# Performance work log

Hardware: AMD Instinct MI355X
Metric: run time of the kernel (lower is better)

Reference implementation:

```python
import jax, jax.numpy as jnp
import numpy as np

NEG_SLOPE = 0.2
EPS = 1e-16  # PyG softmax denominator epsilon


def gat_conv(x, edge_index, W, a_src, a_dst, bias):
    """PyG GATConv, heads=1, concat=True, add_self_loops=True, edge_dim=None."""
    N = x.shape[0]
    h = x @ W  # [N, d]
    loops = jnp.arange(N)
    src = jnp.concatenate([edge_index[0], loops])  # [E+N]
    dst = jnp.concatenate([edge_index[1], loops])
    # per-node attention dot-products, gathered per edge
    s = h @ a_src  # [N]
    t = h @ a_dst  # [N]
    e = jax.nn.leaky_relu(s[src] + t[dst], NEG_SLOPE)  # [E+N]
    # segment softmax over incoming edges of each dst node
    m = jax.ops.segment_max(e, dst, num_segments=N)
    ex = jnp.exp(e - m[dst])
    denom = jax.ops.segment_sum(ex, dst, num_segments=N)
    alpha = ex / (denom[dst] + EPS)  # [E+N]
    out = jax.ops.segment_sum(h[src] * alpha[:, None], dst, num_segments=N)
    return out + bias


def setup_inputs() -> dict:
    key = jax.random.key(0)
    N, E, D, DE = 50000, 600000, 128, 16
    ks = jax.random.split(key, 12)
    scale = 1.0 / np.sqrt(D)
    return {
        "x_one": jax.random.normal(ks[0], (N, D), jnp.float32),
        "edge_index_one": jax.random.randint(ks[1], (2, E), 0, N, jnp.int64),
        "edge_attr_emb_one": jax.random.normal(ks[2], (E, DE), jnp.float32),
        "x_two": jax.random.normal(ks[3], (N, D), jnp.float32),
        "edge_index_two": jax.random.randint(ks[4], (2, E), 0, N, jnp.int64),
        "edge_attr_emb_two": jax.random.normal(ks[5], (E, DE), jnp.float32),
        "W1": jax.random.normal(ks[6], (D, D), jnp.float32) * scale,
        "a_src1": jax.random.normal(ks[7], (D,), jnp.float32) * scale,
        "a_dst1": jax.random.normal(ks[8], (D,), jnp.float32) * scale,
        "b1": jnp.zeros((D,), jnp.float32),
        "W2": jax.random.normal(ks[9], (D, D), jnp.float32) * scale,
        "a_src2": jax.random.normal(ks[10], (D,), jnp.float32) * scale,
        "a_dst2": jax.random.normal(ks[11], (D,), jnp.float32) * scale,
        "b2": jnp.zeros((D,), jnp.float32),
    }


def reference(x_one, edge_index_one, edge_attr_emb_one,
              x_two, edge_index_two, edge_attr_emb_two,
              W1, a_src1, a_dst1, b1, W2, a_src2, a_dst2, b2):
    # edge_attr is ignored: GATConv was built without edge_dim.
    # F.dropout(training=False) is identity in eval mode.
    out_one = jax.nn.relu(gat_conv(x_one, edge_index_one, W1, a_src1, a_dst1, b1))
    out_two = jax.nn.relu(gat_conv(x_two, edge_index_two, W2, a_src2, a_dst2, b2))
    return (out_one, out_two)
```

## Files before the change

### kernel.cpp

```cpp
#include <hip/hip_runtime.h>
#include <math.h>

#define D 128
#define NEG_SLOPE 0.2f
#define EPS 1e-16f
#define PT 4096
#define SCAP 1024
#define CSRCAP (SCAP + 64)

typedef __attribute__((ext_vector_type(8))) __bf16 bf16x8;
typedef __attribute__((ext_vector_type(4))) float f32x4;
typedef __attribute__((ext_vector_type(2))) float f32x2;

__device__ __forceinline__ unsigned short f2bf(float f) {
    return __builtin_bit_cast(unsigned short, (__bf16)f);
}
__device__ __forceinline__ unsigned long long pack4bf(float a, float b, float c, float d) {
    return (unsigned long long)f2bf(a)
         | ((unsigned long long)f2bf(b) << 16)
         | ((unsigned long long)f2bf(c) << 32)
         | ((unsigned long long)f2bf(d) << 48);
}
__device__ __forceinline__ f32x2 bf2f2(unsigned u) {
    f32x2 r;
    r.x = __uint_as_float(u << 16);
    r.y = __uint_as_float(u & 0xffff0000u);
    return r;
}

__global__ __launch_bounds__(256) void k_gemm(const float* __restrict__ X0,
                                              const float* __restrict__ X1,
                                              const float* __restrict__ W0,
                                              const float* __restrict__ W1,
                                              const float* __restrict__ as0,
                                              const float* __restrict__ as1,
                                              const float* __restrict__ ad0,
                                              const float* __restrict__ ad1,
                                              unsigned short* __restrict__ Hb,
                                              float* __restrict__ sv,
                                              float* __restrict__ tv, int N, int nb) {
    __shared__ char lds[65536];
    const int t = threadIdx.x;
    const int g = (blockIdx.x >= nb) ? 1 : 0;
    const int row0 = (blockIdx.x - g * nb) * 128;
    const float* X = g ? X1 : X0;
    const float* W = g ? W1 : W0;
    const float* a_src = g ? as1 : as0;
    const float* a_dst = g ? ad1 : ad0;
    const int gbase = g * N;

    {
        const int n = t & 127;
        const int khalf = (t >> 7) * 64;
        #pragma unroll 4
        for (int i = 0; i < 16; ++i) {
            const int k0 = khalf + i * 4;
            float f0 = W[(size_t)(k0 + 0) * D + n];
            float f1 = W[(size_t)(k0 + 1) * D + n];
            float f2 = W[(size_t)(k0 + 2) * D + n];
            float f3 = W[(size_t)(k0 + 3) * D + n];
            int off = (n * 256 + k0 * 2) ^ ((n & 7) << 4);
            *(unsigned long long*)(lds + 32768 + off) = pack4bf(f0, f1, f2, f3);
        }
    }
    {
        const int c = t & 31;
        #pragma unroll 4
        for (int p = 0; p < 16; ++p) {
            const int m = p * 8 + (t >> 5);
            const int gr = row0 + m;
            float4 v = make_float4(0.f, 0.f, 0.f, 0.f);
            if (gr < N) v = ((const float4*)X)[(size_t)gr * 32 + c];
            int off = (m * 256 + c * 8) ^ ((m & 7) << 4);
            *(unsigned long long*)(lds + off) = pack4bf(v.x, v.y, v.z, v.w);
        }
    }
    __syncthreads();

    const int w = t >> 6;
    const int l = t & 63;
    const int lr = l & 15;
    const int lg = l >> 4;

    f32x4 acc[2][8];
    #pragma unroll
    for (int r = 0; r < 2; ++r)
        #pragma unroll
        for (int nt = 0; nt < 8; ++nt) acc[r][nt] = (f32x4){0.f, 0.f, 0.f, 0.f};

    #pragma unroll
    for (int kk = 0; kk < 4; ++kk) {
        const int kByte = kk * 64 + lg * 16;
        const int m0 = w * 32 + lr;
        const int m1 = m0 + 16;
        bf16x8 a0 = *(const bf16x8*)(lds + ((m0 * 256 + kByte) ^ ((m0 & 7) << 4)));
        bf16x8 a1 = *(const bf16x8*)(lds + ((m1 * 256 + kByte) ^ ((m1 & 7) << 4)));
        #pragma unroll
        for (int nt = 0; nt < 8; ++nt) {
            const int n = nt * 16 + lr;
            bf16x8 b = *(const bf16x8*)(lds + 32768 + ((n * 256 + kByte) ^ ((n & 7) << 4)));
            acc[0][nt] = __builtin_amdgcn_mfma_f32_16x16x32_bf16(a0, b, acc[0][nt], 0, 0, 0);
            acc[1][nt] = __builtin_amdgcn_mfma_f32_16x16x32_bf16(a1, b, acc[1][nt], 0, 0, 0);
        }
    }

    float asv[8], adv[8];
    #pragma unroll
    for (int nt = 0; nt < 8; ++nt) {
        asv[nt] = a_src[nt * 16 + lr];
        adv[nt] = a_dst[nt * 16 + lr];
    }
    #pragma unroll
    for (int r = 0; r < 2; ++r) {
        #pragma unroll
        for (int reg = 0; reg < 4; ++reg) {
            const int row = row0 + w * 32 + r * 16 + lg * 4 + reg;
            float ss = 0.f, tt = 0.f;
            #pragma unroll
            for (int nt = 0; nt < 8; ++nt) {
                float hv = acc[r][nt][reg];
                ss += hv * asv[nt];
                tt += hv * adv[nt];
                if (row < N) Hb[(size_t)(gbase + row) * D + nt * 16 + lr] = f2bf(hv);
            }
            #pragma unroll
            for (int off = 8; off; off >>= 1) {
                ss += __shfl_xor(ss, off);
                tt += __shfl_xor(tt, off);
            }
            if (lr == 0 && row < N) { sv[gbase + row] = ss; tv[gbase + row] = tt; }
        }
    }
}

__global__ __launch_bounds__(256) void k_fill(int* __restrict__ fill, int NSB) {
    int i = blockIdx.x * 256 + threadIdx.x;
    if (i < NSB) fill[i] = i * SCAP;
}

__global__ __launch_bounds__(256) void k_part(const int* __restrict__ s0,
                                              const int* __restrict__ d0,
                                              const int* __restrict__ s1,
                                              const int* __restrict__ d1,
                                              int* __restrict__ fill,
                                              unsigned* __restrict__ P,
                                              int E0, int Et, int N, int NSB) {
    __shared__ int hcnt[2048];
    __shared__ int hbase[2048];
    const int t = threadIdx.x;
    const int i0 = blockIdx.x * PT;
    const int i1 = min(i0 + PT, Et);
    for (int i = t; i < NSB; i += 256) hcnt[i] = 0;
    __syncthreads();
    for (int i = i0 + t; i < i1; i += 256) {
        int dd = (i < E0) ? d0[i] : d1[i - E0] + N;
        atomicAdd(&hcnt[dd >> 6], 1);
    }
    __syncthreads();
    for (int i = t; i < NSB; i += 256) {
        int c = hcnt[i];
        hbase[i] = c ? atomicAdd(&fill[i], c) : 0;
        hcnt[i] = 0;
    }
    __syncthreads();
    for (int i = i0 + t; i < i1; i += 256) {
        int ss, dd;
        if (i < E0) { ss = s0[i]; dd = d0[i]; }
        else        { ss = s1[i - E0] + N; dd = d1[i - E0] + N; }
        int sb = dd >> 6;
        int pos = hbase[sb] + atomicAdd(&hcnt[sb], 1);
        if (pos < (sb + 1) * SCAP)
            P[pos] = (unsigned)ss | ((unsigned)(dd & 63) << 26);
    }
}

__global__ __launch_bounds__(256) void k_gatherf(const unsigned* __restrict__ P,
                                                 const int* __restrict__ fill,
                                                 const float* __restrict__ sv,
                                                 const float* __restrict__ tv,
                                                 const unsigned short* __restrict__ Hb,
                                                 const float* __restrict__ b0,
                                                 const float* __restrict__ b1,
                                                 float* __restrict__ out, int N, int M) {
    __shared__ int cnt[64];
    __shared__ int rp[65];
    __shared__ float dsum[64];
    __shared__ float tvl[64];
    __shared__ int cw[CSRCAP];
    __shared__ unsigned short plb[CSRCAP];
    const int t = threadIdx.x;
    const int sb = blockIdx.x;
    const int bstart = sb * SCAP;
    int bend = fill[sb];
    if (bend > bstart + SCAP) bend = bstart + SCAP;
    const int dbase = sb << 6;

    if (t < 64) {
        cnt[t] = 1;
        int d = dbase + t;
        tvl[t] = (d < M) ? tv[d] : 0.f;
    }
    __syncthreads();
    for (int i = bstart + t; i < bend; i += 256)
        atomicAdd(&cnt[(P[i] >> 26) & 63], 1);
    __syncthreads();
    if (t < 64) {
        int v = cnt[t];
        int inc = v;
        #pragma unroll
        for (int off = 1; off < 64; off <<= 1) {
            int x = __shfl_up(inc, off);
            if (t >= off) inc += x;
        }
        rp[t + 1] = inc;
        if (t == 0) rp[0] = 0;
        int st = inc - v;
        cnt[t] = st + 1;
        int d = dbase + t;
        if (d < M) {
            float es = sv[d] + tvl[t];
            es = (es > 0.f) ? es : NEG_SLOPE * es;
            unsigned short pb = f2bf(__expf(es));
            cw[st] = d;
            plb[st] = pb;
            dsum[t] = __uint_as_float((unsigned)pb << 16);
        } else {
            cw[st] = 0;
            plb[st] = 0;
            dsum[t] = 1.f;
        }
    }
    __syncthreads();
    for (int i = bstart + t; i < bend; i += 256) {
        unsigned w = P[i];
        int dlo = (int)(w >> 26) & 63;
        int src = (int)(w & 0x03FFFFFFu);
        float e = sv[src] + tvl[dlo];
        e = (e > 0.f) ? e : NEG_SLOPE * e;
        unsigned short pb = f2bf(__expf(e));
        int pos = atomicAdd(&cnt[dlo], 1);
        cw[pos] = src;
        plb[pos] = pb;
        atomicAdd(&dsum[dlo], __uint_as_float((unsigned)pb << 16));
    }
    __syncthreads();

    const int wv = t >> 6;
    const int lane = t & 63;
    const int qtr = lane >> 4;
    const int sl = lane & 15;

    for (int q = 0; q < 16; ++q) {
        const int ld = wv * 16 + q;
        const int d = dbase + ld;
        if (d >= M) break;
        const int start = rp[ld];
        const int dg = rp[ld + 1] - start;

        f32x2 a0 = {0.f, 0.f}, a1 = {0.f, 0.f}, a2 = {0.f, 0.f}, a3 = {0.f, 0.f};
        int j = qtr;
        for (; j + 12 < dg; j += 16) {
            const int e0 = start + j;
            int sA = cw[e0];
            int sB = cw[e0 + 4];
            int sC = cw[e0 + 8];
            int sD = cw[e0 + 12];
            float pA = __uint_as_float((unsigned)plb[e0] << 16);
            float pB = __uint_as_float((unsigned)plb[e0 + 4] << 16);
            float pC = __uint_as_float((unsigned)plb[e0 + 8] << 16);
            float pD = __uint_as_float((unsigned)plb[e0 + 12] << 16);
            uint4 wA = *(const uint4*)(Hb + (size_t)sA * D + sl * 8);
            uint4 wB = *(const uint4*)(Hb + (size_t)sB * D + sl * 8);
            uint4 wC = *(const uint4*)(Hb + (size_t)sC * D + sl * 8);
            uint4 wD = *(const uint4*)(Hb + (size_t)sD * D + sl * 8);
            a0 += pA * bf2f2(wA.x); a1 += pA * bf2f2(wA.y); a2 += pA * bf2f2(wA.z); a3 += pA * bf2f2(wA.w);
            a0 += pB * bf2f2(wB.x); a1 += pB * bf2f2(wB.y); a2 += pB * bf2f2(wB.z); a3 += pB * bf2f2(wB.w);
            a0 += pC * bf2f2(wC.x); a1 += pC * bf2f2(wC.y); a2 += pC * bf2f2(wC.z); a3 += pC * bf2f2(wC.w);
            a0 += pD * bf2f2(wD.x); a1 += pD * bf2f2(wD.y); a2 += pD * bf2f2(wD.z); a3 += pD * bf2f2(wD.w);
        }
        for (; j < dg; j += 4) {
            const int e0 = start + j;
            int sA = cw[e0];
            float pA = __uint_as_float((unsigned)plb[e0] << 16);
            uint4 wA = *(const uint4*)(Hb + (size_t)sA * D + sl * 8);
            a0 += pA * bf2f2(wA.x); a1 += pA * bf2f2(wA.y); a2 += pA * bf2f2(wA.z); a3 += pA * bf2f2(wA.w);
        }

        #pragma unroll
        for (int off = 16; off <= 32; off <<= 1) {
            a0.x += __shfl_xor(a0.x, off); a0.y += __shfl_xor(a0.y, off);
            a1.x += __shfl_xor(a1.x, off); a1.y += __shfl_xor(a1.y, off);
            a2.x += __shfl_xor(a2.x, off); a2.y += __shfl_xor(a2.y, off);
            a3.x += __shfl_xor(a3.x, off); a3.y += __shfl_xor(a3.y, off);
        }

        if (qtr == 0) {
            const float* bp = ((d < N) ? b0 : b1) + sl * 8;
            float inv = 1.0f / (dsum[ld] + EPS);
            float4 o0, o1;
            o0.x = fmaxf(a0.x * inv + bp[0], 0.f);
            o0.y = fmaxf(a0.y * inv + bp[1], 0.f);
            o0.z = fmaxf(a1.x * inv + bp[2], 0.f);
            o0.w = fmaxf(a1.y * inv + bp[3], 0.f);
            o1.x = fmaxf(a2.x * inv + bp[4], 0.f);
            o1.y = fmaxf(a2.y * inv + bp[5], 0.f);
            o1.z = fmaxf(a3.x * inv + bp[6], 0.f);
            o1.w = fmaxf(a3.y * inv + bp[7], 0.f);
            float4* op = (float4*)(out + (size_t)d * D + sl * 8);
            op[0] = o0;
            op[1] = o1;
        }
    }
}

static inline size_t rup(size_t x) { return (x + 255) & ~(size_t)255; }

extern "C" void kernel_launch(void* const* d_in, const int* in_sizes, int n_in,
                              void* d_out, int out_size, void* d_ws, size_t ws_size,
                              hipStream_t stream) {
    const int N = in_sizes[0] / D;
    const int M = 2 * N;
    const int E0 = in_sizes[1] / 2;
    const int E1 = in_sizes[4] / 2;
    const int Et = E0 + E1;
    const int NSB = (M + 63) >> 6;
    float* out = (float*)d_out;

    char* ws = (char*)d_ws;
    unsigned short* Hb = (unsigned short*)ws; ws += rup((size_t)M * D * sizeof(unsigned short));
    float* sv = (float*)ws;       ws += rup((size_t)M * sizeof(float));
    float* tv = (float*)ws;       ws += rup((size_t)M * sizeof(float));
    int* fill = (int*)ws;         ws += rup((size_t)NSB * sizeof(int));
    unsigned* P = (unsigned*)ws;

    const int* EI0 = (const int*)d_in[1];
    const int* EI1 = (const int*)d_in[4];
    const int* s0 = EI0, *d0 = EI0 + E0;
    const int* s1 = EI1, *d1 = EI1 + E1;

    const int nb = (N + 127) / 128;

    k_gemm<<<2 * nb, 256, 0, stream>>>((const float*)d_in[0], (const float*)d_in[3],
                                       (const float*)d_in[6], (const float*)d_in[10],
                                       (const float*)d_in[7], (const float*)d_in[11],
                                       (const float*)d_in[8], (const float*)d_in[12],
                                       Hb, sv, tv, N, nb);
    k_fill<<<(NSB + 255) / 256, 256, 0, stream>>>(fill, NSB);
    k_part<<<(Et + PT - 1) / PT, 256, 0, stream>>>(s0, d0, s1, d1, fill, P, E0, Et, N, NSB);
    k_gatherf<<<NSB, 256, 0, stream>>>(P, fill, sv, tv, Hb,
                                       (const float*)d_in[9], (const float*)d_in[13],
                                       out, N, M);
}
```

Baseline: 119.3 us.

## Halve destination buckets, fuse fill into GEMM, pack fp32 edge weights

Destination super-buckets shrink from 64 to 32 nodes with half the capacity, which doubles the number of gather blocks (more parallelism and less LDS per block). The partition tile grows to 8192 edges, so fewer k_part blocks each do more atomic base reservations. The separate fill-init kernel is folded into the GEMM kernel, removing one launch. Edge source index and weight are now packed together as fp32 uint2 in LDS instead of bf16-rounded weights in a separate array. The exchange is more LDS traffic per edge, and the smaller 512-entry buckets can overflow for high in-degree nodes.

```diff
diff --git a/kernel.cpp b/kernel.cpp
--- a/kernel.cpp
+++ b/kernel.cpp
@@ -4,9 +4,10 @@
 #define D 128
 #define NEG_SLOPE 0.2f
 #define EPS 1e-16f
-#define PT 4096
-#define SCAP 1024
-#define CSRCAP (SCAP + 64)
+#define PT 8192
+#define SBSH 5
+#define SCAP 512
+#define CSRCAP (SCAP + 32)
 
 typedef __attribute__((ext_vector_type(8))) __bf16 bf16x8;
 typedef __attribute__((ext_vector_type(4))) float f32x4;
@@ -38,9 +39,15 @@
                                               const float* __restrict__ ad1,
                                               unsigned short* __restrict__ Hb,
                                               float* __restrict__ sv,
-                                              float* __restrict__ tv, int N, int nb) {
+                                              float* __restrict__ tv,
+                                              int* __restrict__ fill,
+                                              int N, int nb, int NSB) {
     __shared__ char lds[65536];
     const int t = threadIdx.x;
+    {
+        int gi = blockIdx.x * 256 + t;
+        if (gi < NSB) fill[gi] = gi * SCAP;
+    }
     const int g = (blockIdx.x >= nb) ? 1 : 0;
     const int row0 = (blockIdx.x - g * nb) * 128;
     const float* X = g ? X1 : X0;
@@ -133,11 +140,6 @@
     }
 }
 
-__global__ __launch_bounds__(256) void k_fill(int* __restrict__ fill, int NSB) {
-    int i = blockIdx.x * 256 + threadIdx.x;
-    if (i < NSB) fill[i] = i * SCAP;
-}
-
 __global__ __launch_bounds__(256) void k_part(const int* __restrict__ s0,
                                               const int* __restrict__ d0,
                                               const int* __restrict__ s1,
@@ -145,8 +147,8 @@
                                               int* __restrict__ fill,
                                               unsigned* __restrict__ P,
                                               int E0, int Et, int N, int NSB) {
-    __shared__ int hcnt[2048];
-    __shared__ int hbase[2048];
+    __shared__ int hcnt[3200];
+    __shared__ int hbase[3200];
     const int t = threadIdx.x;
     const int i0 = blockIdx.x * PT;
     const int i1 = min(i0 + PT, Et);
@@ -154,7 +156,7 @@
     __syncthreads();
     for (int i = i0 + t; i < i1; i += 256) {
         int dd = (i < E0) ? d0[i] : d1[i - E0] + N;
-        atomicAdd(&hcnt[dd >> 6], 1);
+        atomicAdd(&hcnt[dd >> SBSH], 1);
     }
     __syncthreads();
     for (int i = t; i < NSB; i += 256) {
@@ -167,10 +169,10 @@
         int ss, dd;
         if (i < E0) { ss = s0[i]; dd = d0[i]; }
         else        { ss = s1[i - E0] + N; dd = d1[i - E0] + N; }
-        int sb = dd >> 6;
+        int sb = dd >> SBSH;
         int pos = hbase[sb] + atomicAdd(&hcnt[sb], 1);
         if (pos < (sb + 1) * SCAP)
-            P[pos] = (unsigned)ss | ((unsigned)(dd & 63) << 26);
+            P[pos] = (unsigned)ss | ((unsigned)(dd & 31) << 27);
     }
 }
 
@@ -182,33 +184,32 @@
                                                  const float* __restrict__ b0,
                                                  const float* __restrict__ b1,
                                                  float* __restrict__ out, int N, int M) {
-    __shared__ int cnt[64];
-    __shared__ int rp[65];
-    __shared__ float dsum[64];
-    __shared__ float tvl[64];
-    __shared__ int cw[CSRCAP];
-    __shared__ unsigned short plb[CSRCAP];
+    __shared__ int cnt[32];
+    __shared__ int rp[33];
+    __shared__ float dsum[32];
+    __shared__ float tvl[32];
+    __shared__ uint2 ep[CSRCAP];
     const int t = threadIdx.x;
     const int sb = blockIdx.x;
     const int bstart = sb * SCAP;
     int bend = fill[sb];
     if (bend > bstart + SCAP) bend = bstart + SCAP;
-    const int dbase = sb << 6;
-
-    if (t < 64) {
+    const int dbase = sb << SBSH;
+
+    if (t < 32) {
         cnt[t] = 1;
         int d = dbase + t;
         tvl[t] = (d < M) ? tv[d] : 0.f;
     }
     __syncthreads();
     for (int i = bstart + t; i < bend; i += 256)
-        atomicAdd(&cnt[(P[i] >> 26) & 63], 1);
-    __syncthreads();
-    if (t < 64) {
+        atomicAdd(&cnt[P[i] >> 27], 1);
+    __syncthreads();
+    if (t < 32) {
         int v = cnt[t];
         int inc = v;
         #pragma unroll
-        for (int off = 1; off < 64; off <<= 1) {
+        for (int off = 1; off < 32; off <<= 1) {
             int x = __shfl_up(inc, off);
             if (t >= off) inc += x;
         }
@@ -220,28 +221,25 @@
         if (d < M) {
             float es = sv[d] + tvl[t];
             es = (es > 0.f) ? es : NEG_SLOPE * es;
-            unsigned short pb = f2bf(__expf(es));
-            cw[st] = d;
-            plb[st] = pb;
-            dsum[t] = __uint_as_float((unsigned)pb << 16);
+            float ps = __expf(es);
+            ep[st] = make_uint2((unsigned)d, __float_as_uint(ps));
+            dsum[t] = ps;
         } else {
-            cw[st] = 0;
-            plb[st] = 0;
+            ep[st] = make_uint2(0u, 0u);
             dsum[t] = 1.f;
         }
     }
     __syncthreads();
     for (int i = bstart + t; i < bend; i += 256) {
         unsigned w = P[i];
-        int dlo = (int)(w >> 26) & 63;
-        int src = (int)(w & 0x03FFFFFFu);
+        int dlo = (int)(w >> 27);
+        int src = (int)(w & 0x07FFFFFFu);
         float e = sv[src] + tvl[dlo];
         e = (e > 0.f) ? e : NEG_SLOPE * e;
-        unsigned short pb = f2bf(__expf(e));
+        float p = __expf(e);
         int pos = atomicAdd(&cnt[dlo], 1);
-        cw[pos] = src;
-        plb[pos] = pb;
-        atomicAdd(&dsum[dlo], __uint_as_float((unsigned)pb << 16));
+        ep[pos] = make_uint2((unsigned)src, __float_as_uint(p));
+        atomicAdd(&dsum[dlo], p);
     }
     __syncthreads();
 
@@ -250,8 +248,8 @@
     const int qtr = lane >> 4;
     const int sl = lane & 15;
 
-    for (int q = 0; q < 16; ++q) {
-        const int ld = wv * 16 + q;
+    for (int q = 0; q < 8; ++q) {
+        const int ld = wv * 8 + q;
         const int d = dbase + ld;
         if (d >= M) break;
         const int start = rp[ld];
@@ -261,18 +259,18 @@
         int j = qtr;
         for (; j + 12 < dg; j += 16) {
             const int e0 = start + j;
-            int sA = cw[e0];
-            int sB = cw[e0 + 4];
-            int sC = cw[e0 + 8];
-            int sD = cw[e0 + 12];
-            float pA = __uint_as_float((unsigned)plb[e0] << 16);
-            float pB = __uint_as_float((unsigned)plb[e0 + 4] << 16);
-            float pC = __uint_as_float((unsigned)plb[e0 + 8] << 16);
-            float pD = __uint_as_float((unsigned)plb[e0 + 12] << 16);
-            uint4 wA = *(const uint4*)(Hb + (size_t)sA * D + sl * 8);
-            uint4 wB = *(const uint4*)(Hb + (size_t)sB * D + sl * 8);
-            uint4 wC = *(const uint4*)(Hb + (size_t)sC * D + sl * 8);
-            uint4 wD = *(const uint4*)(Hb + (size_t)sD * D + sl * 8);
+            uint2 eA = ep[e0];
+            uint2 eB = ep[e0 + 4];
+            uint2 eC = ep[e0 + 8];
+            uint2 eD = ep[e0 + 12];
+            float pA = __uint_as_float(eA.y);
+            float pB = __uint_as_float(eB.y);
+            float pC = __uint_as_float(eC.y);
+            float pD = __uint_as_float(eD.y);
+            uint4 wA = *(const uint4*)(Hb + (size_t)eA.x * D + sl * 8);
+            uint4 wB = *(const uint4*)(Hb + (size_t)eB.x * D + sl * 8);
+            uint4 wC = *(const uint4*)(Hb + (size_t)eC.x * D + sl * 8);
+            uint4 wD = *(const uint4*)(Hb + (size_t)eD.x * D + sl * 8);
             a0 += pA * bf2f2(wA.x); a1 += pA * bf2f2(wA.y); a2 += pA * bf2f2(wA.z); a3 += pA * bf2f2(wA.w);
             a0 += pB * bf2f2(wB.x); a1 += pB * bf2f2(wB.y); a2 += pB * bf2f2(wB.z); a3 += pB * bf2f2(wB.w);
             a0 += pC * bf2f2(wC.x); a1 += pC * bf2f2(wC.y); a2 += pC * bf2f2(wC.z); a3 += pC * bf2f2(wC.w);
@@ -280,9 +278,9 @@
         }
         for (; j < dg; j += 4) {
             const int e0 = start + j;
-            int sA = cw[e0];
-            float pA = __uint_as_float((unsigned)plb[e0] << 16);
-            uint4 wA = *(const uint4*)(Hb + (size_t)sA * D + sl * 8);
+            uint2 eA = ep[e0];
+            float pA = __uint_as_float(eA.y);
+            uint4 wA = *(const uint4*)(Hb + (size_t)eA.x * D + sl * 8);
             a0 += pA * bf2f2(wA.x); a1 += pA * bf2f2(wA.y); a2 += pA * bf2f2(wA.z); a3 += pA * bf2f2(wA.w);
         }
 
@@ -323,7 +321,7 @@
     const int E0 = in_sizes[1] / 2;
     const int E1 = in_sizes[4] / 2;
     const int Et = E0 + E1;
-    const int NSB = (M + 63) >> 6;
+    const int NSB = (M + 31) >> SBSH;
     float* out = (float*)d_out;
 
     char* ws = (char*)d_ws;
@@ -344,8 +342,7 @@
                                        (const float*)d_in[6], (const float*)d_in[10],
                                        (const float*)d_in[7], (const float*)d_in[11],
                                        (const float*)d_in[8], (const float*)d_in[12],
-                                       Hb, sv, tv, N, nb);
-    k_fill<<<(NSB + 255) / 256, 256, 0, stream>>>(fill, NSB);
+                                       Hb, sv, tv, fill, N, nb, NSB);
     k_part<<<(Et + PT - 1) / PT, 256, 0, stream>>>(s0, d0, s1, d1, fill, P, E0, Et, N, NSB);
     k_gatherf<<<NSB, 256, 0, stream>>>(P, fill, sv, tv, Hb,
                                        (const float*)d_in[9], (const float*)d_in[13],
```

Measured after the change: 124.2 us. 4.2% more time.
